# Performance work log

Hardware: AMD Instinct MI355X
Metric: run time of the kernel (lower is better)

The kernel has to match this reference:

```python
import jax, jax.numpy as jnp
import numpy as np
from jax import lax

IN_CH, OUT_CH, K, STYLE_DIM = 512, 512, 3, 512
B, H, W = 16, 64, 64
SCALE = 1.0 / np.sqrt(IN_CH * K * K).astype(np.float32)
EPS = 1e-8


def setup_inputs() -> dict:
    key = jax.random.key(0)
    k1, k2, k3, k4 = jax.random.split(key, 4)
    return {
        "x": jax.random.normal(k1, (B, IN_CH, H, W), dtype=jnp.float32),
        "style": jax.random.normal(k2, (B, STYLE_DIM), dtype=jnp.float32),
        "weight": jax.random.normal(k3, (1, OUT_CH, IN_CH, K, K), dtype=jnp.float32),
        "mod_w": jax.random.normal(k4, (IN_CH, STYLE_DIM), dtype=jnp.float32) / np.sqrt(STYLE_DIM),
        "mod_b": jnp.ones((IN_CH,), dtype=jnp.float32),
    }


def reference(x, style, weight, mod_w, mod_b):
    b, cin, h, w = x.shape
    out_ch = weight.shape[1]
    k = weight.shape[-1]
    pad = k // 2
    # style projection: (B, in_channel)
    s = style @ mod_w.T + mod_b
    # modulated weight: (B, out, in, k, k)
    wmod = SCALE * weight * s[:, None, :, None, None]
    # demodulation: rsqrt of sum of squares over (in, kh, kw)
    demod = lax.rsqrt(jnp.sum(wmod * wmod, axis=(2, 3, 4)) + EPS)
    wmod = wmod * demod[:, :, None, None, None]
    # grouped conv with groups = batch
    wflat = wmod.reshape(b * out_ch, cin, k, k)
    xin = x.reshape(1, b * cin, h, w)
    out = lax.conv_general_dilated(
        xin, wflat,
        window_strides=(1, 1),
        padding=[(pad, pad), (pad, pad)],
        dimension_numbers=("NCHW", "OIHW", "NCHW"),
        feature_group_count=b,
    )
    return out.reshape(b, out_ch, h, w)
```

## Files before the change

kernel.cpp:

```cpp
#include <hip/hip_runtime.h>
#include <hip/hip_bf16.h>
#include <cstdint>
#include <cstddef>

typedef __bf16 bf16x8 __attribute__((ext_vector_type(8)));
typedef float f32x4 __attribute__((ext_vector_type(4)));
typedef float f32x16 __attribute__((ext_vector_type(16)));

#define MOD_SCALE 1.4731391e-02f
#define EPSF 1e-8f

__global__ __launch_bounds__(512) void k_style(
    const float* __restrict__ style, const float* __restrict__ mod_w,
    const float* __restrict__ mod_b, float* __restrict__ s)
{
  __shared__ float st[512];
  const int b = blockIdx.x, i = threadIdx.x;
  st[i] = style[b*512 + i];
  __syncthreads();
  const float4* mw = (const float4*)(mod_w + (size_t)i*512);
  float acc = 0.f;
  #pragma unroll 8
  for (int j = 0; j < 128; ++j) {
    float4 v = mw[j];
    acc += v.x*st[4*j] + v.y*st[4*j+1] + v.z*st[4*j+2] + v.w*st[4*j+3];
  }
  s[b*512 + i] = acc + mod_b[i];
}

__global__ __launch_bounds__(256) void k_weight(
    const float* __restrict__ weight, float* __restrict__ w2,
    __hip_bfloat16* __restrict__ Wb)
{
  const int o = blockIdx.x, t = threadIdx.x;
  #pragma unroll
  for (int h = 0; h < 2; ++h) {
    const int i = t + h*256;
    const float* wp = weight + ((size_t)o*512 + i)*9;
    float sq = 0.f;
    #pragma unroll
    for (int kk = 0; kk < 9; ++kk) {
      float v = wp[kk];
      sq += v*v;
      Wb[((size_t)kk*512 + o)*512 + i] = __float2bfloat16(v * MOD_SCALE);
    }
    w2[(size_t)o*512 + i] = sq;
  }
}

__global__ __launch_bounds__(256) void k_demod(
    const float* __restrict__ s, const float* __restrict__ w2,
    float* __restrict__ demod)
{
  __shared__ float s2[512];
  const int b = blockIdx.x, t = threadIdx.x;
  {
    float a = s[b*512 + t];        s2[t]     = a*a;
    float c = s[b*512 + t + 256];  s2[t+256] = c*c;
  }
  __syncthreads();
  #pragma unroll
  for (int h = 0; h < 2; ++h) {
    const int o = t + h*256;
    const float4* wp = (const float4*)(w2 + (size_t)o*512);
    float acc = 0.f;
    #pragma unroll 8
    for (int j = 0; j < 128; ++j) {
      float4 v = wp[j];
      acc += v.x*s2[4*j] + v.y*s2[4*j+1] + v.z*s2[4*j+2] + v.w*s2[4*j+3];
    }
    demod[b*512 + o] = rsqrtf(MOD_SCALE*MOD_SCALE*acc + EPSF);
  }
}

__global__ __launch_bounds__(256) void k_xm(
    const float* __restrict__ x, const float* __restrict__ s,
    __hip_bfloat16* __restrict__ Xm)
{
  __shared__ __hip_bfloat16 T[64][40];
  const int bid = blockIdx.x;
  const int cb = bid & 15, y = (bid >> 4) & 63, b = bid >> 10;
  const int ic0 = cb*32;
  const int t = threadIdx.x;
  const int i = t >> 3, x0 = (t & 7)*8;
  const float sv = s[b*512 + ic0 + i];
  const float4* xp = (const float4*)(x + (size_t)(b*512 + ic0 + i)*4096 + y*64 + x0);
  float4 v0 = xp[0], v1 = xp[1];
  float vals[8] = {v0.x, v0.y, v0.z, v0.w, v1.x, v1.y, v1.z, v1.w};
  #pragma unroll
  for (int j = 0; j < 8; ++j) T[x0+j][i] = __float2bfloat16(vals[j]*sv);

  const float4 z4 = make_float4(0.f, 0.f, 0.f, 0.f);
  if (t < 8) {
    const int side = t >> 2, j = t & 3;
    float4* hz = (float4*)(Xm + (((size_t)(b*66 + (y+1))*66 + side*65)*512 + ic0 + j*8));
    *hz = z4;
  }
  if (y == 0) {
    for (int idx = t; idx < 264; idx += 256) {
      const int px = idx >> 2, j = idx & 3;
      float4* hz = (float4*)(Xm + (((size_t)(b*66 + 0)*66 + px)*512 + ic0 + j*8));
      *hz = z4;
    }
  }
  if (y == 63) {
    for (int idx = t; idx < 264; idx += 256) {
      const int px = idx >> 2, j = idx & 3;
      float4* hz = (float4*)(Xm + (((size_t)(b*66 + 65)*66 + px)*512 + ic0 + j*8));
      *hz = z4;
    }
  }

  __syncthreads();
  const int p = t >> 2, c = (t & 3)*8;
  __hip_bfloat16* dst = Xm + (((size_t)(b*66 + (y+1))*66 + (p+1))*512 + ic0 + c);
  *(float4*)dst = *(const float4*)&T[p][c];
}

#define VMC(n) asm volatile("s_waitcnt vmcnt(" #n ")" ::: "memory")

__global__ __launch_bounds__(512, 2) void k_conv(
    const __hip_bfloat16* __restrict__ Wb,
    const __hip_bfloat16* __restrict__ Xm,
    const float* __restrict__ demod,
    float* __restrict__ out)
{
  __shared__ __hip_bfloat16 lds[2][2][16384];

  const int orig = blockIdx.x;
  const int swz = (orig & 7)*64 + (orig >> 3);
  const int b  = swz >> 5;
  const int nt = (swz & 31) >> 1;
  const int mt = swz & 1;
  const int o0 = mt*256, y0 = nt*4;

  const int tid = threadIdx.x;
  const int l = tid & 63;
  const int w = tid >> 6;
  const int wm = w >> 2;
  const int wn = w & 3;

  const int srow = tid >> 3;
  const int tq   = (tid & 7) ^ (srow & 7);
  const char* WbC = (const char*)Wb;
  const char* XmC = (const char*)Xm;

  const int rowb = ((l >> 5) << 4) | (l & 15);
  const int lb4  = (l >> 4) & 1;
  const int sB   = (l & 7) << 4;

  #define STAGE_A(tau, h, bfi) do { \
    const int kk_ = (tau) >> 3; \
    const int cb_ = ((tau) & 7) << 7; \
    _Pragma("unroll") \
    for (int it_ = 0; it_ < 2; ++it_) { \
      const int R_ = it_*64 + srow; \
      const int gr_ = (R_ & 0x6F) | ((tq & 1) << 4); \
      const int gc_ = ((tq & 6) | ((R_ >> 4) & 1)) << 4; \
      const char* src_ = WbC + (size_t)(kk_*512 + o0 + (h)*128 + gr_)*1024 + cb_ + gc_; \
      __builtin_amdgcn_global_load_lds( \
        (__attribute__((address_space(1))) void*)src_, \
        (__attribute__((address_space(3))) void*)((char*)&lds[bfi][0][0] + (h)*16384 + it_*8192 + w*1024), \
        16, 0, 0); \
    } \
  } while(0)

  #define STAGE_B(tau, h, bfi) do { \
    const int kk_ = (tau) >> 3; \
    const int cb_ = ((tau) & 7) << 7; \
    const int dy_ = kk_/3 - 1, dx_ = kk_ - (kk_/3)*3 - 1; \
    _Pragma("unroll") \
    for (int it_ = 0; it_ < 2; ++it_) { \
      const int R_ = it_*64 + srow; \
      const int gr_ = (R_ & 0x6F) | ((tq & 1) << 4); \
      const int gc_ = ((tq & 6) | ((R_ >> 4) & 1)) << 4; \
      const int py_ = y0 + (h)*2 + (gr_ >> 6) + dy_ + 1; \
      const int px_ = (gr_ & 63) + dx_ + 1; \
      const char* src_ = XmC + ((size_t)((b*66 + py_)*66 + px_))*1024 + cb_ + gc_; \
      __builtin_amdgcn_global_load_lds( \
        (__attribute__((address_space(1))) void*)src_, \
        (__attribute__((address_space(3))) void*)((char*)&lds[bfi][1][0] + (h)*16384 + it_*8192 + w*1024), \
        16, 0, 0); \
    } \
  } while(0)

  #define RD_A(Ab, MH, dst) do { \
    _Pragma("unroll") \
    for (int mi_ = 0; mi_ < 2; ++mi_) \
      _Pragma("unroll") \
      for (int ks_ = 0; ks_ < 4; ++ks_) \
        dst[mi_][ks_] = *(const bf16x8*)((Ab) + (MH)*16384 + wm*8192 + mi_*4096 \
            + rowb*128 + (((((ks_<<1)|lb4)) << 4) ^ sB)); \
  } while(0)

  #define RD_B(Bb, NH, dst) do { \
    _Pragma("unroll") \
    for (int ks_ = 0; ks_ < 4; ++ks_) \
      dst[ks_] = *(const bf16x8*)((Bb) + (NH)*16384 + wn*4096 \
          + rowb*128 + (((((ks_<<1)|lb4)) << 4) ^ sB)); \
  } while(0)

  #define MFMAQ(AM0, dstA, NH, dstB) do { \
    _Pragma("unroll") \
    for (int ks_ = 0; ks_ < 4; ++ks_) \
      _Pragma("unroll") \
      for (int mi_ = 0; mi_ < 2; ++mi_) \
        acc[(AM0)+mi_][NH] = __builtin_amdgcn_mfma_f32_32x32x16_bf16( \
            dstA[mi_][ks_], dstB[ks_], acc[(AM0)+mi_][NH], 0, 0, 0); \
  } while(0)

  #define TILE(BFI, S1, S2, S3, S4, VM1, VM4) do { \
    const char* Ab_ = (const char*)&lds[BFI][0][0]; \
    const char* Bb_ = (const char*)&lds[BFI][1][0]; \
    bf16x8 a0_[2][4], a1_[2][4], b0_[4], b1_[4]; \
     \
    RD_A(Ab_, 0, a0_); RD_B(Bb_, 0, b0_); \
    S1; \
    __builtin_amdgcn_s_barrier(); \
    __builtin_amdgcn_s_setprio(1); MFMAQ(0, a0_, 0, b0_); __builtin_amdgcn_s_setprio(0); \
    VM1; \
    __builtin_amdgcn_s_barrier(); \
     \
    RD_B(Bb_, 1, b1_); \
    S2; \
    __builtin_amdgcn_s_barrier(); \
    __builtin_amdgcn_s_setprio(1); MFMAQ(0, a0_, 1, b1_); __builtin_amdgcn_s_setprio(0); \
    __builtin_amdgcn_s_barrier(); \
     \
    RD_A(Ab_, 1, a1_); \
    S3; \
    __builtin_amdgcn_s_barrier(); \
    __builtin_amdgcn_s_setprio(1); MFMAQ(2, a1_, 1, b1_); __builtin_amdgcn_s_setprio(0); \
    __builtin_amdgcn_s_barrier(); \
     \
    S4; \
    __builtin_amdgcn_s_barrier(); \
    __builtin_amdgcn_s_setprio(1); MFMAQ(2, a1_, 0, b0_); __builtin_amdgcn_s_setprio(0); \
    VM4; \
    __builtin_amdgcn_s_barrier(); \
  } while(0)

  f32x16 acc[4][2] = {};

  STAGE_A(0, 0, 0); STAGE_A(0, 1, 0); STAGE_B(0, 0, 0); STAGE_B(0, 1, 0);
  STAGE_B(1, 0, 1); STAGE_A(1, 1, 1);
  VMC(4);
  __builtin_amdgcn_s_barrier();

  #pragma unroll 1
  for (int tt = 0; tt < 35; ++tt) {
    const int t = tt*2;
    TILE(0, STAGE_A(t+1,0,1), STAGE_B(t+1,1,1), STAGE_B(t+2,0,0), STAGE_A(t+2,1,0),
            VMC(6), VMC(6));
    TILE(1, STAGE_A(t+2,0,0), STAGE_B(t+2,1,0), STAGE_B(t+3,0,1), STAGE_A(t+3,1,1),
            VMC(6), VMC(6));
  }
  TILE(0, STAGE_A(71,0,1), STAGE_B(71,1,1), (void)0, (void)0, VMC(6), VMC(2));
  TILE(1, (void)0, (void)0, (void)0, (void)0, VMC(0), (void)0);

  const int lr = l & 31;
  #pragma unroll
  for (int am = 0; am < 4; ++am) {
    const int om = o0 + (am >> 1)*128 + wm*64 + (am & 1)*32 + ((l >> 5) << 2);
    #pragma unroll
    for (int NH = 0; NH < 2; ++NH) {
      const int nc = NH*128 + wn*32 + lr;
      const int y = y0 + (nc >> 6), xx = nc & 63;
      #pragma unroll
      for (int g = 0; g < 4; ++g) {
        const f32x4 dm = *(const f32x4*)(demod + b*512 + om + 8*g);
        float* op = out + (size_t)(b*512 + om + 8*g)*4096 + y*64 + xx;
        #pragma unroll
        for (int j = 0; j < 4; ++j)
          op[(size_t)j*4096] = acc[am][NH][g*4 + j] * dm[j];
      }
    }
  }
  #undef TILE
  #undef MFMAQ
  #undef RD_A
  #undef RD_B
  #undef STAGE_A
  #undef STAGE_B
}

extern "C" void kernel_launch(void* const* d_in, const int* in_sizes, int n_in,
                              void* d_out, int out_size, void* d_ws, size_t ws_size,
                              hipStream_t stream)
{
  const float* x      = (const float*)d_in[0];
  const float* style  = (const float*)d_in[1];
  const float* weight = (const float*)d_in[2];
  const float* mod_w  = (const float*)d_in[3];
  const float* mod_b  = (const float*)d_in[4];
  float* out = (float*)d_out;

  char* ws = (char*)d_ws;
  float* s            = (float*)(ws);
  float* demod        = (float*)(ws + 32768);
  float* w2           = (float*)(ws + 65536);
  __hip_bfloat16* Wb  = (__hip_bfloat16*)(ws + 1114112);
  __hip_bfloat16* Xm  = (__hip_bfloat16*)(ws + 5832704);

  k_style <<<16,    512, 0, stream>>>(style, mod_w, mod_b, s);
  k_weight<<<512,   256, 0, stream>>>(weight, w2, Wb);
  k_demod <<<16,    256, 0, stream>>>(s, w2, demod);
  k_xm    <<<16384, 256, 0, stream>>>(x, s, Xm);
  k_conv  <<<512,   512, 0, stream>>>(Wb, Xm, demod, out);
}
```

Baseline: 391.2 us.

## Replace 8-phase ping-pong schedule with simple double-buffered tile loop

Replaces the fine-grained four-quarter tile schedule, which interleaved staging of the next tiles with MFMA quarters and used several barriers per tile, with a simpler loop. Each tile now issues all global-to-LDS loads for the next tile up front, then runs four k-steps that read A and B fragments and issue eight MFMAs each, then waits for all loads and barriers once. This cuts barrier count and staging depth to one tile ahead, at the cost of less overlap and a full vmcnt(0) wait each tile.

```diff
diff --git a/kernel.cpp b/kernel.cpp
--- a/kernel.cpp
+++ b/kernel.cpp
@@ -184,79 +184,53 @@
     } \
   } while(0)
 
-  #define RD_A(Ab, MH, dst) do { \
-    _Pragma("unroll") \
-    for (int mi_ = 0; mi_ < 2; ++mi_) \
-      _Pragma("unroll") \
-      for (int ks_ = 0; ks_ < 4; ++ks_) \
-        dst[mi_][ks_] = *(const bf16x8*)((Ab) + (MH)*16384 + wm*8192 + mi_*4096 \
-            + rowb*128 + (((((ks_<<1)|lb4)) << 4) ^ sB)); \
-  } while(0)
-
-  #define RD_B(Bb, NH, dst) do { \
-    _Pragma("unroll") \
-    for (int ks_ = 0; ks_ < 4; ++ks_) \
-      dst[ks_] = *(const bf16x8*)((Bb) + (NH)*16384 + wn*4096 \
-          + rowb*128 + (((((ks_<<1)|lb4)) << 4) ^ sB)); \
-  } while(0)
-
-  #define MFMAQ(AM0, dstA, NH, dstB) do { \
-    _Pragma("unroll") \
-    for (int ks_ = 0; ks_ < 4; ++ks_) \
-      _Pragma("unroll") \
-      for (int mi_ = 0; mi_ < 2; ++mi_) \
-        acc[(AM0)+mi_][NH] = __builtin_amdgcn_mfma_f32_32x32x16_bf16( \
-            dstA[mi_][ks_], dstB[ks_], acc[(AM0)+mi_][NH], 0, 0, 0); \
-  } while(0)
-
-  #define TILE(BFI, S1, S2, S3, S4, VM1, VM4) do { \
+  #define STAGE_TILE(tau, bfi) do { \
+    STAGE_A(tau, 0, bfi); STAGE_A(tau, 1, bfi); \
+    STAGE_B(tau, 0, bfi); STAGE_B(tau, 1, bfi); \
+  } while(0)
+
+  f32x16 acc[4][2] = {};
+
+  #define TILE(BFI, STG, VMCW, BAR) do { \
     const char* Ab_ = (const char*)&lds[BFI][0][0]; \
     const char* Bb_ = (const char*)&lds[BFI][1][0]; \
-    bf16x8 a0_[2][4], a1_[2][4], b0_[4], b1_[4]; \
-     \
-    RD_A(Ab_, 0, a0_); RD_B(Bb_, 0, b0_); \
-    S1; \
-    __builtin_amdgcn_s_barrier(); \
-    __builtin_amdgcn_s_setprio(1); MFMAQ(0, a0_, 0, b0_); __builtin_amdgcn_s_setprio(0); \
-    VM1; \
-    __builtin_amdgcn_s_barrier(); \
-     \
-    RD_B(Bb_, 1, b1_); \
-    S2; \
-    __builtin_amdgcn_s_barrier(); \
-    __builtin_amdgcn_s_setprio(1); MFMAQ(0, a0_, 1, b1_); __builtin_amdgcn_s_setprio(0); \
-    __builtin_amdgcn_s_barrier(); \
-     \
-    RD_A(Ab_, 1, a1_); \
-    S3; \
-    __builtin_amdgcn_s_barrier(); \
-    __builtin_amdgcn_s_setprio(1); MFMAQ(2, a1_, 1, b1_); __builtin_amdgcn_s_setprio(0); \
-    __builtin_amdgcn_s_barrier(); \
-     \
-    S4; \
-    __builtin_amdgcn_s_barrier(); \
-    __builtin_amdgcn_s_setprio(1); MFMAQ(2, a1_, 0, b0_); __builtin_amdgcn_s_setprio(0); \
-    VM4; \
-    __builtin_amdgcn_s_barrier(); \
-  } while(0)
-
-  f32x16 acc[4][2] = {};
-
-  STAGE_A(0, 0, 0); STAGE_A(0, 1, 0); STAGE_B(0, 0, 0); STAGE_B(0, 1, 0);
-  STAGE_B(1, 0, 1); STAGE_A(1, 1, 1);
-  VMC(4);
+    STG; \
+    _Pragma("unroll") \
+    for (int p_ = 0; p_ < 4; ++p_) { \
+      bf16x8 a_[4], b_[2]; \
+      const int kc_ = (((p_ << 1) | lb4) << 4) ^ sB; \
+      _Pragma("unroll") \
+      for (int j_ = 0; j_ < 4; ++j_) \
+        a_[j_] = *(const bf16x8*)(Ab_ + (j_ >> 1)*16384 + wm*8192 + (j_ & 1)*4096 \
+                                  + rowb*128 + kc_); \
+      _Pragma("unroll") \
+      for (int nh_ = 0; nh_ < 2; ++nh_) \
+        b_[nh_] = *(const bf16x8*)(Bb_ + nh_*16384 + wn*4096 + rowb*128 + kc_); \
+      __builtin_amdgcn_s_setprio(1); \
+      _Pragma("unroll") \
+      for (int j_ = 0; j_ < 4; ++j_) \
+        _Pragma("unroll") \
+        for (int nh_ = 0; nh_ < 2; ++nh_) \
+          acc[j_][nh_] = __builtin_amdgcn_mfma_f32_32x32x16_bf16( \
+              a_[j_], b_[nh_], acc[j_][nh_], 0, 0, 0); \
+      __builtin_amdgcn_s_setprio(0); \
+    } \
+    VMCW; \
+    if (BAR) __builtin_amdgcn_s_barrier(); \
+  } while(0)
+
+  STAGE_TILE(0, 0);
+  VMC(0);
   __builtin_amdgcn_s_barrier();
 
   #pragma unroll 1
   for (int tt = 0; tt < 35; ++tt) {
     const int t = tt*2;
-    TILE(0, STAGE_A(t+1,0,1), STAGE_B(t+1,1,1), STAGE_B(t+2,0,0), STAGE_A(t+2,1,0),
-            VMC(6), VMC(6));
-    TILE(1, STAGE_A(t+2,0,0), STAGE_B(t+2,1,0), STAGE_B(t+3,0,1), STAGE_A(t+3,1,1),
-            VMC(6), VMC(6));
-  }
-  TILE(0, STAGE_A(71,0,1), STAGE_B(71,1,1), (void)0, (void)0, VMC(6), VMC(2));
-  TILE(1, (void)0, (void)0, (void)0, (void)0, VMC(0), (void)0);
+    TILE(0, STAGE_TILE(t+1, 1), VMC(0), 1);
+    TILE(1, STAGE_TILE(t+2, 0), VMC(0), 1);
+  }
+  TILE(0, STAGE_TILE(71, 1), VMC(0), 1);
+  TILE(1, (void)0, (void)0, 0);
 
   const int lr = l & 31;
   #pragma unroll
@@ -277,9 +251,7 @@
     }
   }
   #undef TILE
-  #undef MFMAQ
-  #undef RD_A
-  #undef RD_B
+  #undef STAGE_TILE
   #undef STAGE_A
   #undef STAGE_B
 }
```

New measurement: 391.8 us. Within noise of the previous version (+0.2%).
